# Kernel optimization log

Hardware: AMD Instinct MI355X
Metric: run time of the kernel (lower is better)

The kernel has to match this reference:

```python
import jax, jax.numpy as jnp
import numpy as np

B, T, D, H = 2, 2048, 1024, 16
Dh = D // H
MAX_LEN = 2048


def build_rope_cache(max_len, head_dim):
    theta = 10000.0 ** (-jnp.arange(0, head_dim, 2, dtype=jnp.float32) / head_dim)
    pos = jnp.arange(max_len, dtype=jnp.float32)
    angles = pos[:, None] * theta[None, :]          # [T, Dh/2]
    sin = jnp.sin(angles)[:, None, :]               # [T, 1, Dh/2]
    cos = jnp.cos(angles)[:, None, :]
    return sin, cos


def apply_rotary_pos_emb(q, k, sin, cos):
    q1, q2 = jnp.split(q, 2, axis=-1)
    k1, k2 = jnp.split(k, 2, axis=-1)
    q_out = jnp.concatenate([q1 * cos + q2 * sin, -q1 * sin + q2 * cos], axis=-1)
    k_out = jnp.concatenate([k1 * cos + k2 * sin, -k1 * sin + k2 * cos], axis=-1)
    return q_out, k_out


def setup_inputs() -> dict:
    key = jax.random.key(0)
    k1, k2, k3 = jax.random.split(key, 3)
    x = jax.random.normal(k1, (B, T, D), dtype=jnp.float32)
    W_qkv = jax.random.normal(k2, (D, 3 * D), dtype=jnp.float32) * (D ** -0.5)
    W_proj = jax.random.normal(k3, (D, D), dtype=jnp.float32) * (D ** -0.5)
    # causal mask: 1.0 where attention is disallowed (future positions)
    mask = jnp.triu(jnp.ones((T, T), dtype=jnp.float32), k=1)
    return {"x": x, "mask": mask, "W_qkv": W_qkv, "W_proj": W_proj}


def reference(x, mask, W_qkv, W_proj):
    b, t, d = x.shape
    qkv = x @ W_qkv                                  # [B,T,3D]
    q, k, v = jnp.split(qkv, 3, axis=-1)
    q = q.reshape(b, t, H, Dh)
    k = k.reshape(b, t, H, Dh)
    v = v.reshape(b, t, H, Dh)
    sin, cos = build_rope_cache(MAX_LEN, Dh)
    q, k = apply_rotary_pos_emb(q, k, sin[:t], cos[:t])
    scale = 1.0 / jnp.sqrt(jnp.float32(Dh))
    att = jnp.einsum('bthd,bThd->bhtT', q, k) * scale
    att = att + mask * -1e9                          # mask broadcasts [T,T]->[B,H,T,T]
    weights = jax.nn.softmax(att, axis=-1)
    out = jnp.einsum('bhtT,bThd->bthd', weights, v).reshape(b, t, d)
    return out @ W_proj
```

## Files before the change

kernel.cpp:

```cpp
#include <hip/hip_runtime.h>
#include <hip/hip_bf16.h>

typedef __bf16  bf16x8 __attribute__((ext_vector_type(8)));
typedef __bf16  bf16x4 __attribute__((ext_vector_type(4)));
typedef __bf16  bf16x2 __attribute__((ext_vector_type(2)));
typedef float   f32x4  __attribute__((ext_vector_type(4)));
typedef float   f32x16 __attribute__((ext_vector_type(16)));
typedef unsigned u32x4 __attribute__((ext_vector_type(4)));

#define MFMA16(a,b,c) __builtin_amdgcn_mfma_f32_16x16x32_bf16(a,b,c,0,0,0)
#define MFMA32(a,b,c) __builtin_amdgcn_mfma_f32_32x32x16_bf16(a,b,c,0,0,0)


struct bf4 { __hip_bfloat16 a,b,c,d; };

__global__ __launch_bounds__(256) void prep(const float* __restrict__ x,
                                            const float* __restrict__ Wqkv,
                                            const float* __restrict__ Wproj,
                                            __hip_bfloat16* __restrict__ xb,
                                            __hip_bfloat16* __restrict__ Wqt,
                                            __hip_bfloat16* __restrict__ Wpt,
                                            float2* __restrict__ tbl) {
  __shared__ float tile[32][33];
  int bid = blockIdx.x;
  if (bid < 4096) {
    int i = bid * 256 + threadIdx.x;
    float4 v = ((const float4*)x)[i];
    bf4 o { __float2bfloat16(v.x), __float2bfloat16(v.y),
            __float2bfloat16(v.z), __float2bfloat16(v.w) };
    ((bf4*)xb)[i] = o;
  } else if (bid < 8192) {
    const float* W; __hip_bfloat16* WT; int R, C, bx, by;
    if (bid < 7168) { int e = bid - 4096; W = Wqkv;  WT = Wqt; R = 1024; C = 3072; bx = e % 96; by = e / 96; }
    else            { int e = bid - 7168; W = Wproj; WT = Wpt; R = 1024; C = 1024; bx = e % 32; by = e / 32; }
    int c0 = bx * 32, r0 = by * 32;
    int tx = threadIdx.x & 31, ty = threadIdx.x >> 5;
    #pragma unroll
    for (int i = 0; i < 32; i += 8)
      tile[ty + i][tx] = W[(size_t)(r0 + ty + i) * C + c0 + tx];
    __syncthreads();
    #pragma unroll
    for (int i = 0; i < 32; i += 8)
      WT[(size_t)(c0 + ty + i) * R + r0 + tx] = __float2bfloat16(tile[tx][ty + i]);
  } else {
    int idx = (bid - 8192) * 256 + threadIdx.x;
    int i = idx & 31, t = idx >> 5;
    float theta = expf(-9.210340371976184f * (float)i * 0.03125f);
    float sn, cs;
    sincosf((float)t * theta, &sn, &cs);
    tbl[idx] = float2{sn, cs};
  }
}

__global__ __launch_bounds__(256) void gemm_qkv(const __hip_bfloat16* __restrict__ A,
                                                const __hip_bfloat16* __restrict__ BT,
                                                const float2* __restrict__ tbl,
                                                __hip_bfloat16* __restrict__ Qb,
                                                __hip_bfloat16* __restrict__ Kb,
                                                __hip_bfloat16* __restrict__ Vt) {
  __shared__ __align__(16) char smem[34816];
  auto As = (__hip_bfloat16 (*)[128][32])(smem);
  auto Bs = (__hip_bfloat16 (*)[128][32])(smem + 16384);
  auto Vl = (__hip_bfloat16 (*)[136])(smem);
  const int K = 1024;
  int tid  = threadIdx.x;
  int lane = tid & 63, wid = tid >> 6;
  int wm = wid >> 1, wn = wid & 1;
  int rowBase = blockIdx.y * 128;
  int colBase = blockIdx.x * 128;
  int lr = lane & 15, lg = lane >> 4;

  f32x4 acc[4][4];
  #pragma unroll
  for (int i = 0; i < 4; ++i)
    #pragma unroll
    for (int j = 0; j < 4; ++j) acc[i][j] = f32x4{0.f,0.f,0.f,0.f};

  int nt = K >> 5;

#define GSTAGE(buf, kt)                                                                 \
  do {                                                                                  \
    int k0_ = (kt) << 5;                                                                \
    _Pragma("unroll")                                                                   \
    for (int p = 0; p < 2; ++p) {                                                       \
      int idx = p * 256 + tid;                                                          \
      int r_ = idx >> 2, sl_ = idx & 3;                                                 \
      __builtin_amdgcn_global_load_lds(                                                 \
        (const __attribute__((address_space(1))) unsigned int*)                         \
          &A[(size_t)(rowBase + r_) * K + k0_ + ((sl_ ^ (r_ & 3)) * 8)],                \
        (__attribute__((address_space(3))) unsigned int*)&As[buf][r_][sl_ * 8], 16, 0, 0);\
      __builtin_amdgcn_global_load_lds(                                                 \
        (const __attribute__((address_space(1))) unsigned int*)                         \
          &BT[(size_t)(colBase + r_) * K + k0_ + ((sl_ ^ (r_ & 3)) * 8)],               \
        (__attribute__((address_space(3))) unsigned int*)&Bs[buf][r_][sl_ * 8], 16, 0, 0);\
    }                                                                                   \
  } while (0)

  GSTAGE(0, 0);
  for (int t = 0; t < nt; ++t) {
    int cur = t & 1;
    if (t + 1 < nt) {
      GSTAGE(cur ^ 1, t + 1);
      asm volatile("s_waitcnt vmcnt(4)" ::: "memory");
    } else {
      asm volatile("s_waitcnt vmcnt(0)" ::: "memory");
    }
    __builtin_amdgcn_s_barrier();
    __builtin_amdgcn_sched_barrier(0);

    bf16x8 af[4], bfr[4];
    #pragma unroll
    for (int mf = 0; mf < 4; ++mf) {
      int row = wm*64 + mf*16 + lr;
      af[mf]  = *(const bf16x8*)&As[cur][row][((lg ^ (lr & 3)) * 8)];
    }
    #pragma unroll
    for (int nf = 0; nf < 4; ++nf) {
      int row = wn*64 + nf*16 + lr;
      bfr[nf] = *(const bf16x8*)&Bs[cur][row][((lg ^ (lr & 3)) * 8)];
    }
    #pragma unroll
    for (int mf = 0; mf < 4; ++mf)
      #pragma unroll
      for (int nf = 0; nf < 4; ++nf)
        acc[mf][nf] = MFMA16(af[mf], bfr[nf], acc[mf][nf]);

    __builtin_amdgcn_s_barrier();
  }
#undef GSTAGE

  int region = colBase >> 10;
  int b = rowBase >> 11;
  if (region < 2) {
    const float QS = 0.18033688011112042f;
    __hip_bfloat16* dst = (region == 0) ? Qb : Kb;
    float scale = (region == 0) ? QS : 1.0f;
    int h = ((colBase & 1023) >> 6) + wn;
    #pragma unroll
    for (int mf = 0; mf < 4; ++mf)
      #pragma unroll
      for (int r = 0; r < 4; ++r) {
        int row = rowBase + wm*64 + mf*16 + lg*4 + r;
        int t = row & 2047;
        #pragma unroll
        for (int nf = 0; nf < 2; ++nf) {
          int i = nf*16 + lr;
          float2 sc = tbl[(t << 5) + i];
          float v1 = acc[mf][nf][r], v2 = acc[mf][nf+2][r];
          size_t base = ((size_t)((b*16 + h) * 2048 + t)) * 64;
          dst[base + i]      = __float2bfloat16(( v1*sc.y + v2*sc.x) * scale);
          dst[base + 32 + i] = __float2bfloat16((-v1*sc.x + v2*sc.y) * scale);
        }
      }
  } else {
    #pragma unroll
    for (int nf = 0; nf < 4; ++nf) {
      int d = wn*64 + nf*16 + lr;
      #pragma unroll
      for (int mf = 0; mf < 4; ++mf) {
        bf16x4 w;
        #pragma unroll
        for (int r = 0; r < 4; ++r) w[r] = (__bf16)acc[mf][nf][r];
        *(bf16x4*)&Vl[d][wm*64 + mf*16 + lg*4] = w;
      }
    }
    __syncthreads();
    int vd = tid >> 1, half = tid & 1;
    int h = ((colBase - 2048) >> 6) + (vd >> 6);
    int dloc = vd & 63;
    __hip_bfloat16* dstp = Vt + ((size_t)(b*16 + h) * 64 + dloc) * 2048
                              + (rowBase & 2047) + half*64;
    const __hip_bfloat16* srcp = &Vl[vd][half*64];
    #pragma unroll
    for (int g = 0; g < 8; ++g)
      *(bf16x8*)&dstp[g*8] = *(const bf16x8*)&srcp[g*8];
  }
}

__global__ __launch_bounds__(256) void gemm_proj(const __hip_bfloat16* __restrict__ A,
                                                 const __hip_bfloat16* __restrict__ BT,
                                                 float* __restrict__ C,
                                                 int M, int N, int K) {
  __shared__ __hip_bfloat16 As[2][128][32];
  __shared__ __hip_bfloat16 Bs[2][64][32];
  int tid  = threadIdx.x;
  int lane = tid & 63, wid = tid >> 6;
  int wm = wid >> 1, wn = wid & 1;
  int rowBase = blockIdx.y * 128;
  int colBase = blockIdx.x * 64;
  int lr = lane & 15, lg = lane >> 4;

  f32x4 acc[4][2];
  #pragma unroll
  for (int i = 0; i < 4; ++i)
    #pragma unroll
    for (int j = 0; j < 2; ++j) acc[i][j] = f32x4{0.f,0.f,0.f,0.f};

  int nt = K >> 5;

#define PSTAGE(buf, kt)                                                                 \
  do {                                                                                  \
    int k0_ = (kt) << 5;                                                                \
    _Pragma("unroll")                                                                   \
    for (int p = 0; p < 2; ++p) {                                                       \
      int idx = p * 256 + tid;                                                          \
      int r_ = idx >> 2, sl_ = idx & 3;                                                 \
      __builtin_amdgcn_global_load_lds(                                                 \
        (const __attribute__((address_space(1))) unsigned int*)                         \
          &A[(size_t)(rowBase + r_) * K + k0_ + ((sl_ ^ (r_ & 3)) * 8)],                \
        (__attribute__((address_space(3))) unsigned int*)&As[buf][r_][sl_ * 8], 16, 0, 0);\
    }                                                                                   \
    {                                                                                   \
      int r_ = tid >> 2, sl_ = tid & 3;                                                 \
      __builtin_amdgcn_global_load_lds(                                                 \
        (const __attribute__((address_space(1))) unsigned int*)                         \
          &BT[(size_t)(colBase + r_) * K + k0_ + ((sl_ ^ (r_ & 3)) * 8)],               \
        (__attribute__((address_space(3))) unsigned int*)&Bs[buf][r_][sl_ * 8], 16, 0, 0);\
    }                                                                                   \
  } while (0)

  PSTAGE(0, 0);
  for (int t = 0; t < nt; ++t) {
    int cur = t & 1;
    if (t + 1 < nt) {
      PSTAGE(cur ^ 1, t + 1);
      asm volatile("s_waitcnt vmcnt(3)" ::: "memory");
    } else {
      asm volatile("s_waitcnt vmcnt(0)" ::: "memory");
    }
    __builtin_amdgcn_s_barrier();
    __builtin_amdgcn_sched_barrier(0);

    bf16x8 af[4], bfr[2];
    #pragma unroll
    for (int mf = 0; mf < 4; ++mf) {
      int row = wm*64 + mf*16 + lr;
      af[mf]  = *(const bf16x8*)&As[cur][row][((lg ^ (lr & 3)) * 8)];
    }
    #pragma unroll
    for (int nf = 0; nf < 2; ++nf) {
      int row = wn*32 + nf*16 + lr;
      bfr[nf] = *(const bf16x8*)&Bs[cur][row][((lg ^ (lr & 3)) * 8)];
    }
    #pragma unroll
    for (int mf = 0; mf < 4; ++mf)
      #pragma unroll
      for (int nf = 0; nf < 2; ++nf)
        acc[mf][nf] = MFMA16(af[mf], bfr[nf], acc[mf][nf]);

    __builtin_amdgcn_s_barrier();
  }
#undef PSTAGE

  #pragma unroll
  for (int mf = 0; mf < 4; ++mf)
    #pragma unroll
    for (int nf = 0; nf < 2; ++nf)
      #pragma unroll
      for (int r = 0; r < 4; ++r) {
        int row = rowBase + wm*64 + mf*16 + lg*4 + r;
        int col = colBase + wn*32 + nf*16 + lr;
        C[(size_t)row * N + col] = acc[mf][nf][r];
      }
}

__device__ __forceinline__ unsigned pk2(float lo, float hi_) {
  bf16x2 t; t[0] = (__bf16)lo; t[1] = (__bf16)hi_;
  return __builtin_bit_cast(unsigned, t);
}

__global__ __launch_bounds__(512) void attn_chunk(const __hip_bfloat16* __restrict__ Qb,
                                                  const __hip_bfloat16* __restrict__ Kb,
                                                  const __hip_bfloat16* __restrict__ Vt,
                                                  __hip_bfloat16* __restrict__ Opart,
                                                  float* __restrict__ sbuf) {
  __shared__ __hip_bfloat16 Ks[2][2048];
  __shared__ __hip_bfloat16 Vs[2][2048];
  int tid = threadIdx.x;
  int wid = tid >> 6, lane = tid & 63;
  int ql = lane & 31, hi = lane >> 5;

  int bid = blockIdx.x;
  int bh, c, jbase, lenmax; bool diag;
  if (bid < 384) {
    bh = bid / 12; int pr = bid % 12;
    if (pr < 6)       { c = 0; jbase = 16 + 8*pr; }
    else if (pr < 10) { c = 1; jbase = 32 + 8*(pr-6); }
    else              { c = 2; jbase = 48 + 8*(pr-10); }
    lenmax = 16; diag = false;
  } else {
    int e = bid - 384;
    int hh = (e < 128) ? 1 : 0;
    int e2 = e & 127;
    bh = e2 >> 2; c = e2 & 3;
    jbase = 16*c + 8*hh; lenmax = 8*hh + 8; diag = true;
  }
  int j = jbase + wid;
  int len = diag ? ((j & 15) + 1) : 16;
  int q0 = j * 32, t0 = c * 512;
  int jobid;
  if (!diag) jobid = (c == 0) ? (j - 16) : ((c == 1) ? (j + 16) : (j + 32));
  else       jobid = 96 + ((15 - (j & 15)) << 2) + c;
  int job = jobid * 32 + bh;

  const __hip_bfloat16* Qp = Qb + (size_t)bh * 2048 * 64;
  const __hip_bfloat16* Kp = Kb + (size_t)bh * 2048 * 64;
  const __hip_bfloat16* Vp = Vt + (size_t)bh * 64 * 2048;

  bf16x8 qf[4];
  #pragma unroll
  for (int cc = 0; cc < 4; ++cc)
    qf[cc] = *(const bf16x8*)&Qp[(size_t)(q0 + ql) * 64 + cc*16 + hi*8];

  f32x16 o0, o1;
  #pragma unroll
  for (int r = 0; r < 16; ++r) { o0[r] = 0.f; o1[r] = 0.f; }
  float s = 0.f;

  int kr = tid >> 3, ksl = tid & 7;
  int vjj = tid - 256;
  int ve  = (vjj >> 4) & 1;
  int vx  = vjj ^ (ve << 2);
  int vr  = vx >> 2;
  int vtc = (vx & 3) ^ (vr & 3);

#define ASTAGE(buf, it_)                                                                \
  do {                                                                                  \
    int kv0_ = t0 + (it_) * 32;                                                         \
    if (tid < 256)                                                                      \
      __builtin_amdgcn_global_load_lds(                                                 \
        (const __attribute__((address_space(1))) unsigned int*)                         \
          &Kp[(size_t)(kv0_ + kr) * 64 + ((ksl ^ (kr & 7)) * 8)],                       \
        (__attribute__((address_space(3))) unsigned int*)&Ks[buf][tid * 8], 16, 0, 0);  \
    else                                                                                \
      __builtin_amdgcn_global_load_lds(                                                 \
        (const __attribute__((address_space(1))) unsigned int*)                         \
          &Vp[(size_t)vr * 2048 + kv0_ + vtc * 8],                                      \
        (__attribute__((address_space(3))) unsigned int*)&Vs[buf][vjj * 8], 16, 0, 0);  \
  } while (0)

  ASTAGE(0, 0);
  for (int it = 0; it < lenmax; ++it) {
    int cur = it & 1;
    if (it + 1 < lenmax) {
      ASTAGE(cur ^ 1, it + 1);
      asm volatile("s_waitcnt vmcnt(1)" ::: "memory");
    } else {
      asm volatile("s_waitcnt vmcnt(0)" ::: "memory");
    }
    __builtin_amdgcn_s_barrier();
    __builtin_amdgcn_sched_barrier(0);

    if (it < len) {
      int kv0 = t0 + it * 32;
      bf16x8 kf[4], vf[4];
      #pragma unroll
      for (int cc = 0; cc < 4; ++cc)
        kf[cc] = *(const bf16x8*)&Ks[cur][ql * 64 + (((cc*2 + hi) ^ (ql & 7)) * 8)];
      #pragma unroll
      for (int g = 0; g < 2; ++g)
        #pragma unroll
        for (int cc = 0; cc < 2; ++cc) {
          int d_ = g*32 + ql, tc_ = cc*2 + hi;
          int L = (d_*4 + (tc_ ^ (d_ & 3))) ^ (((d_ >> 2) & 1) << 2);
          vf[g*2 + cc] = *(const bf16x8*)&Vs[cur][L * 8];
        }

      f32x16 st;
      #pragma unroll
      for (int r = 0; r < 16; ++r) st[r] = 0.f;
      #pragma unroll
      for (int cc = 0; cc < 4; ++cc) st = MFMA32(kf[cc], qf[cc], st);

      if (diag && it == len - 1) {
        #pragma unroll
        for (int r = 0; r < 16; ++r) {
          int kv = kv0 + (r & 3) + 8*(r >> 2) + 4*hi;
          if (kv > q0 + ql) st[r] = -1e30f;
        }
      }

      float p[16]; float ps = 0.f;
      #pragma unroll
      for (int r = 0; r < 16; ++r) { p[r] = exp2f(st[r]); ps += p[r]; }
      ps += __shfl_xor(ps, 32);
      s += ps;

      bf16x8 pb[2];
      #pragma unroll
      for (int cc = 0; cc < 2; ++cc) {
        unsigned w0 = pk2(p[cc*8+0], p[cc*8+1]);
        unsigned w1 = pk2(p[cc*8+2], p[cc*8+3]);
        unsigned w2 = pk2(p[cc*8+4], p[cc*8+5]);
        unsigned w3 = pk2(p[cc*8+6], p[cc*8+7]);
        unsigned r0 = __shfl_xor(hi ? w0 : w2, 32);
        unsigned r1 = __shfl_xor(hi ? w1 : w3, 32);
        u32x4 pw;
        pw[0] = hi ? r0 : w0;
        pw[1] = hi ? r1 : w1;
        pw[2] = hi ? w2 : r0;
        pw[3] = hi ? w3 : r1;
        pb[cc] = __builtin_bit_cast(bf16x8, pw);
      }

      o0 = MFMA32(vf[0], pb[0], o0);
      o0 = MFMA32(vf[1], pb[1], o0);
      o1 = MFMA32(vf[2], pb[0], o1);
      o1 = MFMA32(vf[3], pb[1], o1);
    }
    __builtin_amdgcn_s_barrier();
  }
#undef ASTAGE

  __hip_bfloat16* Op = Opart + (size_t)job * 2048 + ql * 64;
  #pragma unroll
  for (int rr = 0; rr < 4; ++rr) {
    bf16x4 w;
    #pragma unroll
    for (int e = 0; e < 4; ++e) w[e] = (__bf16)o0[rr*4 + e];
    *(bf16x4*)&Op[8*rr + 4*hi] = w;
  }
  #pragma unroll
  for (int rr = 0; rr < 4; ++rr) {
    bf16x4 w;
    #pragma unroll
    for (int e = 0; e < 4; ++e) w[e] = (__bf16)o1[rr*4 + e];
    *(bf16x4*)&Op[32 + 8*rr + 4*hi] = w;
  }
  if (hi == 0) sbuf[(size_t)job * 32 + ql] = s;
}

__global__ __launch_bounds__(64) void attn_combine(const __hip_bfloat16* __restrict__ Opart,
                                                   const float* __restrict__ sbuf,
                                                   __hip_bfloat16* __restrict__ Ob) {
  int bid2 = blockIdx.x;
  int j = bid2 >> 5, bh = bid2 & 31;
  int h = bh & 15, b = bh >> 4;
  int tid = threadIdx.x, ql = tid & 31, half = tid >> 5;
  int nc = (j >> 4) + 1;

  int gs[4];
  const int Sseg[3] = {0, 48, 80};
  #pragma unroll
  for (int i = 0; i < 3; ++i)
    if (i < nc - 1) gs[i] = (Sseg[i] + j - 16*(i+1)) * 32 + bh;
  gs[nc-1] = (96 + 4*(15 - (j & 15)) + (j >> 4)) * 32 + bh;

  float Ssum = 0.f;
  #pragma unroll
  for (int i = 0; i < 4; ++i)
    if (i < nc) Ssum += sbuf[(size_t)gs[i]*32 + ql];

  float acc[32];
  #pragma unroll
  for (int e = 0; e < 32; ++e) acc[e] = 0.f;
  #pragma unroll
  for (int i = 0; i < 4; ++i)
    if (i < nc) {
      const bf16x8* src = (const bf16x8*)(Opart + (size_t)gs[i]*2048 + ql*64 + half*32);
      #pragma unroll
      for (int q4 = 0; q4 < 4; ++q4) {
        bf16x8 v = src[q4];
        #pragma unroll
        for (int e = 0; e < 8; ++e) acc[q4*8 + e] += (float)v[e];
      }
    }

  float inv = 1.f / Ssum;
  size_t row = (size_t)b * 2048 + j*32 + ql;
  __hip_bfloat16* dst = Ob + row * 1024 + h*64 + half*32;
  #pragma unroll
  for (int q4 = 0; q4 < 4; ++q4) {
    bf16x8 w;
    #pragma unroll
    for (int e = 0; e < 8; ++e) w[e] = (__bf16)(acc[q4*8 + e] * inv);
    *(bf16x8*)&dst[q4*8] = w;
  }
}

extern "C" void kernel_launch(void* const* d_in, const int* in_sizes, int n_in,
                              void* d_out, int out_size, void* d_ws, size_t ws_size,
                              hipStream_t stream) {
  const float* x     = (const float*)d_in[0];
  const float* Wqkv  = (const float*)d_in[2];
  const float* Wproj = (const float*)d_in[3];
  float* out = (float*)d_out;

  char* ws = (char*)d_ws;
  const size_t MB = 1024 * 1024;
  __hip_bfloat16* xb  = (__hip_bfloat16*)(ws);
  __hip_bfloat16* Wqt = (__hip_bfloat16*)(ws +  8*MB);
  __hip_bfloat16* Wpt = (__hip_bfloat16*)(ws + 14*MB);
  __hip_bfloat16* Qb  = (__hip_bfloat16*)(ws + 40*MB);
  __hip_bfloat16* Kb  = (__hip_bfloat16*)(ws + 48*MB);
  __hip_bfloat16* Vt  = (__hip_bfloat16*)(ws + 56*MB);
  __hip_bfloat16* Ob  = (__hip_bfloat16*)(ws + 64*MB);
  __hip_bfloat16* Opart = (__hip_bfloat16*)(ws + 16*MB);
  float*          sbuf  = (float*)(ws + 36*MB);
  float2*         sctbl = (float2*)(ws + 37*MB);

  prep<<<8448, 256, 0, stream>>>(x, Wqkv, Wproj, xb, Wqt, Wpt, sctbl);
  gemm_qkv<<<dim3(24, 32), 256, 0, stream>>>(xb, Wqt, sctbl, Qb, Kb, Vt);
  attn_chunk<<<640, 512, 0, stream>>>(Qb, Kb, Vt, Opart, sbuf);
  attn_combine<<<2048, 64, 0, stream>>>(Opart, sbuf, Ob);
  gemm_proj<<<dim3(16, 32), 256, 0, stream>>>(Ob, Wpt, out, 4096, 1024, 1024);
}
```

Baseline: 115.1 us.

## Merge paired diagonal attention blocks so each block processes two query tiles

Diagonal chunk blocks previously came in two flavours, covering the upper and lower halves of query tiles with separate K/V loads. Now each diagonal block makes each wave handle two query tiles (j and j-8) against the same staged K/V chunk. This shares K/V loads and cuts the grid from 640 to 512 blocks. A launch-bounds hint of 4 blocks per CU is also added. The cost is twice the accumulator registers in diagonal waves, more per-wave work for those blocks, and possible register pressure under the occupancy hint.

```diff
diff --git a/kernel.cpp b/kernel.cpp
--- a/kernel.cpp
+++ b/kernel.cpp
@@ -269,53 +269,139 @@
   return __builtin_bit_cast(unsigned, t);
 }
 
-__global__ __launch_bounds__(512) void attn_chunk(const __hip_bfloat16* __restrict__ Qb,
-                                                  const __hip_bfloat16* __restrict__ Kb,
-                                                  const __hip_bfloat16* __restrict__ Vt,
-                                                  __hip_bfloat16* __restrict__ Opart,
-                                                  float* __restrict__ sbuf) {
+__device__ __forceinline__ void attn_tile(const __hip_bfloat16* KsB, const __hip_bfloat16* VsB,
+                                          const bf16x8* qf, f32x16& o0, f32x16& o1, float& s,
+                                          int q0, int ql, int hib, int kv0, bool mask) {
+  bf16x8 kf[4], vf[4];
+  #pragma unroll
+  for (int cc = 0; cc < 4; ++cc)
+    kf[cc] = *(const bf16x8*)&KsB[ql * 64 + (((cc*2 + hib) ^ (ql & 7)) * 8)];
+  #pragma unroll
+  for (int g = 0; g < 2; ++g)
+    #pragma unroll
+    for (int cc = 0; cc < 2; ++cc) {
+      int d_ = g*32 + ql, tc_ = cc*2 + hib;
+      int L = (d_*4 + (tc_ ^ (d_ & 3))) ^ (((d_ >> 2) & 1) << 2);
+      vf[g*2 + cc] = *(const bf16x8*)&VsB[L * 8];
+    }
+
+  f32x16 st;
+  #pragma unroll
+  for (int r = 0; r < 16; ++r) st[r] = 0.f;
+  #pragma unroll
+  for (int cc = 0; cc < 4; ++cc) st = MFMA32(kf[cc], qf[cc], st);
+
+  if (mask) {
+    #pragma unroll
+    for (int r = 0; r < 16; ++r) {
+      int kv = kv0 + (r & 3) + 8*(r >> 2) + 4*hib;
+      if (kv > q0 + ql) st[r] = -1e30f;
+    }
+  }
+
+  float p[16]; float ps = 0.f;
+  #pragma unroll
+  for (int r = 0; r < 16; ++r) { p[r] = exp2f(st[r]); ps += p[r]; }
+  ps += __shfl_xor(ps, 32);
+  s += ps;
+
+  bf16x8 pb[2];
+  #pragma unroll
+  for (int cc = 0; cc < 2; ++cc) {
+    unsigned w0 = pk2(p[cc*8+0], p[cc*8+1]);
+    unsigned w1 = pk2(p[cc*8+2], p[cc*8+3]);
+    unsigned w2 = pk2(p[cc*8+4], p[cc*8+5]);
+    unsigned w3 = pk2(p[cc*8+6], p[cc*8+7]);
+    unsigned r0 = __shfl_xor(hib ? w0 : w2, 32);
+    unsigned r1 = __shfl_xor(hib ? w1 : w3, 32);
+    u32x4 pw;
+    pw[0] = hib ? r0 : w0;
+    pw[1] = hib ? r1 : w1;
+    pw[2] = hib ? w2 : r0;
+    pw[3] = hib ? w3 : r1;
+    pb[cc] = __builtin_bit_cast(bf16x8, pw);
+  }
+
+  o0 = MFMA32(vf[0], pb[0], o0);
+  o0 = MFMA32(vf[1], pb[1], o0);
+  o1 = MFMA32(vf[2], pb[0], o1);
+  o1 = MFMA32(vf[3], pb[1], o1);
+}
+
+__device__ __forceinline__ void write_part(__hip_bfloat16* __restrict__ Opart,
+                                           float* __restrict__ sbuf, int job,
+                                           const f32x16& o0, const f32x16& o1, float s,
+                                           int ql, int hib) {
+  __hip_bfloat16* Op = Opart + (size_t)job * 2048 + ql * 64;
+  #pragma unroll
+  for (int rr = 0; rr < 4; ++rr) {
+    bf16x4 w;
+    #pragma unroll
+    for (int e = 0; e < 4; ++e) w[e] = (__bf16)o0[rr*4 + e];
+    *(bf16x4*)&Op[8*rr + 4*hib] = w;
+  }
+  #pragma unroll
+  for (int rr = 0; rr < 4; ++rr) {
+    bf16x4 w;
+    #pragma unroll
+    for (int e = 0; e < 4; ++e) w[e] = (__bf16)o1[rr*4 + e];
+    *(bf16x4*)&Op[32 + 8*rr + 4*hib] = w;
+  }
+  if (hib == 0) sbuf[(size_t)job * 32 + ql] = s;
+}
+
+__global__ __launch_bounds__(512, 4) void attn_chunk(const __hip_bfloat16* __restrict__ Qb,
+                                                     const __hip_bfloat16* __restrict__ Kb,
+                                                     const __hip_bfloat16* __restrict__ Vt,
+                                                     __hip_bfloat16* __restrict__ Opart,
+                                                     float* __restrict__ sbuf) {
   __shared__ __hip_bfloat16 Ks[2][2048];
   __shared__ __hip_bfloat16 Vs[2][2048];
   int tid = threadIdx.x;
   int wid = tid >> 6, lane = tid & 63;
-  int ql = lane & 31, hi = lane >> 5;
+  int ql = lane & 31, hib = lane >> 5;
 
   int bid = blockIdx.x;
-  int bh, c, jbase, lenmax; bool diag;
+  int bh, c; bool diag;
+  int j, len, j2 = 0, len2 = 0;
   if (bid < 384) {
     bh = bid / 12; int pr = bid % 12;
+    int jbase;
     if (pr < 6)       { c = 0; jbase = 16 + 8*pr; }
     else if (pr < 10) { c = 1; jbase = 32 + 8*(pr-6); }
     else              { c = 2; jbase = 48 + 8*(pr-10); }
-    lenmax = 16; diag = false;
+    j = jbase + wid; len = 16; diag = false;
   } else {
     int e = bid - 384;
-    int hh = (e < 128) ? 1 : 0;
-    int e2 = e & 127;
-    bh = e2 >> 2; c = e2 & 3;
-    jbase = 16*c + 8*hh; lenmax = 8*hh + 8; diag = true;
-  }
-  int j = jbase + wid;
-  int len = diag ? ((j & 15) + 1) : 16;
-  int q0 = j * 32, t0 = c * 512;
-  int jobid;
-  if (!diag) jobid = (c == 0) ? (j - 16) : ((c == 1) ? (j + 16) : (j + 32));
-  else       jobid = 96 + ((15 - (j & 15)) << 2) + c;
-  int job = jobid * 32 + bh;
+    bh = e >> 2; c = e & 3;
+    j  = 16*c + 8 + wid;  len  = (j  & 15) + 1;
+    j2 = 16*c + wid;      len2 = (j2 & 15) + 1;
+    diag = true;
+  }
+  int q0 = j * 32, q02 = j2 * 32, t0 = c * 512;
+  int jobid = !diag ? ((c == 0) ? (j - 16) : ((c == 1) ? (j + 16) : (j + 32)))
+                    : (96 + ((15 - (j & 15)) << 2) + c);
+  int job  = jobid * 32 + bh;
+  int job2 = (96 + ((15 - (j2 & 15)) << 2) + c) * 32 + bh;
 
   const __hip_bfloat16* Qp = Qb + (size_t)bh * 2048 * 64;
   const __hip_bfloat16* Kp = Kb + (size_t)bh * 2048 * 64;
   const __hip_bfloat16* Vp = Vt + (size_t)bh * 64 * 2048;
 
-  bf16x8 qf[4];
+  bf16x8 qf[4], qf2[4];
   #pragma unroll
   for (int cc = 0; cc < 4; ++cc)
-    qf[cc] = *(const bf16x8*)&Qp[(size_t)(q0 + ql) * 64 + cc*16 + hi*8];
-
-  f32x16 o0, o1;
-  #pragma unroll
-  for (int r = 0; r < 16; ++r) { o0[r] = 0.f; o1[r] = 0.f; }
-  float s = 0.f;
+    qf[cc] = *(const bf16x8*)&Qp[(size_t)(q0 + ql) * 64 + cc*16 + hib*8];
+  if (diag) {
+    #pragma unroll
+    for (int cc = 0; cc < 4; ++cc)
+      qf2[cc] = *(const bf16x8*)&Qp[(size_t)(q02 + ql) * 64 + cc*16 + hib*8];
+  }
+
+  f32x16 o0, o1, o0b, o1b;
+  #pragma unroll
+  for (int r = 0; r < 16; ++r) { o0[r] = 0.f; o1[r] = 0.f; o0b[r] = 0.f; o1b[r] = 0.f; }
+  float s = 0.f, s2 = 0.f;
 
   int kr = tid >> 3, ksl = tid & 7;
   int vjj = tid - 256;
@@ -340,9 +426,9 @@
   } while (0)
 
   ASTAGE(0, 0);
-  for (int it = 0; it < lenmax; ++it) {
+  for (int it = 0; it < 16; ++it) {
     int cur = it & 1;
-    if (it + 1 < lenmax) {
+    if (it + 1 < 16) {
       ASTAGE(cur ^ 1, it + 1);
       asm volatile("s_waitcnt vmcnt(1)" ::: "memory");
     } else {
@@ -351,83 +437,20 @@
     __builtin_amdgcn_s_barrier();
     __builtin_amdgcn_sched_barrier(0);
 
-    if (it < len) {
-      int kv0 = t0 + it * 32;
-      bf16x8 kf[4], vf[4];
-      #pragma unroll
-      for (int cc = 0; cc < 4; ++cc)
-        kf[cc] = *(const bf16x8*)&Ks[cur][ql * 64 + (((cc*2 + hi) ^ (ql & 7)) * 8)];
-      #pragma unroll
-      for (int g = 0; g < 2; ++g)
-        #pragma unroll
-        for (int cc = 0; cc < 2; ++cc) {
-          int d_ = g*32 + ql, tc_ = cc*2 + hi;
-          int L = (d_*4 + (tc_ ^ (d_ & 3))) ^ (((d_ >> 2) & 1) << 2);
-          vf[g*2 + cc] = *(const bf16x8*)&Vs[cur][L * 8];
-        }
-
-      f32x16 st;
-      #pragma unroll
-      for (int r = 0; r < 16; ++r) st[r] = 0.f;
-      #pragma unroll
-      for (int cc = 0; cc < 4; ++cc) st = MFMA32(kf[cc], qf[cc], st);
-
-      if (diag && it == len - 1) {
-        #pragma unroll
-        for (int r = 0; r < 16; ++r) {
-          int kv = kv0 + (r & 3) + 8*(r >> 2) + 4*hi;
-          if (kv > q0 + ql) st[r] = -1e30f;
-        }
-      }
-
-      float p[16]; float ps = 0.f;
-      #pragma unroll
-      for (int r = 0; r < 16; ++r) { p[r] = exp2f(st[r]); ps += p[r]; }
-      ps += __shfl_xor(ps, 32);
-      s += ps;
-
-      bf16x8 pb[2];
-      #pragma unroll
-      for (int cc = 0; cc < 2; ++cc) {
-        unsigned w0 = pk2(p[cc*8+0], p[cc*8+1]);
-        unsigned w1 = pk2(p[cc*8+2], p[cc*8+3]);
-        unsigned w2 = pk2(p[cc*8+4], p[cc*8+5]);
-        unsigned w3 = pk2(p[cc*8+6], p[cc*8+7]);
-        unsigned r0 = __shfl_xor(hi ? w0 : w2, 32);
-        unsigned r1 = __shfl_xor(hi ? w1 : w3, 32);
-        u32x4 pw;
-        pw[0] = hi ? r0 : w0;
-        pw[1] = hi ? r1 : w1;
-        pw[2] = hi ? w2 : r0;
-        pw[3] = hi ? w3 : r1;
-        pb[cc] = __builtin_bit_cast(bf16x8, pw);
-      }
-
-      o0 = MFMA32(vf[0], pb[0], o0);
-      o0 = MFMA32(vf[1], pb[1], o0);
-      o1 = MFMA32(vf[2], pb[0], o1);
-      o1 = MFMA32(vf[3], pb[1], o1);
-    }
+    int kv0 = t0 + it * 32;
+    if (it < len)
+      attn_tile(Ks[cur], Vs[cur], qf, o0, o1, s, q0, ql, hib, kv0,
+                diag && it == len - 1);
+    if (diag && it < len2)
+      attn_tile(Ks[cur], Vs[cur], qf2, o0b, o1b, s2, q02, ql, hib, kv0,
+                it == len2 - 1);
+
     __builtin_amdgcn_s_barrier();
   }
 #undef ASTAGE
 
-  __hip_bfloat16* Op = Opart + (size_t)job * 2048 + ql * 64;
-  #pragma unroll
-  for (int rr = 0; rr < 4; ++rr) {
-    bf16x4 w;
-    #pragma unroll
-    for (int e = 0; e < 4; ++e) w[e] = (__bf16)o0[rr*4 + e];
-    *(bf16x4*)&Op[8*rr + 4*hi] = w;
-  }
-  #pragma unroll
-  for (int rr = 0; rr < 4; ++rr) {
-    bf16x4 w;
-    #pragma unroll
-    for (int e = 0; e < 4; ++e) w[e] = (__bf16)o1[rr*4 + e];
-    *(bf16x4*)&Op[32 + 8*rr + 4*hi] = w;
-  }
-  if (hi == 0) sbuf[(size_t)job * 32 + ql] = s;
+  write_part(Opart, sbuf, job, o0, o1, s, ql, hib);
+  if (diag) write_part(Opart, sbuf, job2, o0b, o1b, s2, ql, hib);
 }
 
 __global__ __launch_bounds__(64) void attn_combine(const __hip_bfloat16* __restrict__ Opart,
@@ -501,7 +524,7 @@
 
   prep<<<8448, 256, 0, stream>>>(x, Wqkv, Wproj, xb, Wqt, Wpt, sctbl);
   gemm_qkv<<<dim3(24, 32), 256, 0, stream>>>(xb, Wqt, sctbl, Qb, Kb, Vt);
-  attn_chunk<<<640, 512, 0, stream>>>(Qb, Kb, Vt, Opart, sbuf);
+  attn_chunk<<<512, 512, 0, stream>>>(Qb, Kb, Vt, Opart, sbuf);
   attn_combine<<<2048, 64, 0, stream>>>(Opart, sbuf, Ob);
   gemm_proj<<<dim3(16, 32), 256, 0, stream>>>(Ob, Wpt, out, 4096, 1024, 1024);
 }
```

Result: slower. 158.7 us (+37.8%).
